# Optimization experiments

Measured on AMD Instinct MI355X. Metric: run time of the kernel, lower is better.

## Reference

```python
import jax, jax.numpy as jnp
import numpy as np


def setup_inputs() -> dict:
    key = jax.random.key(0)
    ks = jax.random.split(key, 7)
    B, N, Fin, Fout = 32, 1024, 64, 64
    s = 1.0 / np.sqrt(Fin)
    return {
        "X": jax.random.normal(ks[0], (B, N, Fin), dtype=jnp.float32),
        "A": jax.random.normal(ks[1], (B, N, N), dtype=jnp.float32),  # unused in forward, kept for signature fidelity
        "W": jax.random.uniform(ks[2], (Fin, Fout), jnp.float32, -s, s),
        "att_W": jax.random.uniform(ks[3], (Fin, Fout), jnp.float32, -s, s),
        "a": jax.random.uniform(ks[4], (Fout, Fout), jnp.float32, -s, s),
        "bias_W": jax.random.uniform(ks[5], (Fout,), jnp.float32, -s, s),
        "self_W": jax.random.uniform(ks[6], (Fin, Fout), jnp.float32, -s, s),
    }


def reference(X, A, W, att_W, a, bias_W, self_W):
    # att_X = X @ att_W : [B, N, Fout]
    att_X = jnp.einsum('bnf,fg->bng', X, att_W)
    # torch einsum 'ij,ajk->ajk' sums `a` over i => per-feature scale a.sum(0)
    scale = jnp.sum(a, axis=0)  # [Fout]
    # Z[b,i,k] = sum_j att_X[b,i,j] * scale[j] * att_X[b,k,j]  -> [B, N, N]
    Z = jnp.einsum('big,bkg->bik', att_X * scale, att_X)
    n = Z.shape[1]
    Z = Z * (1.0 - jnp.eye(n, dtype=Z.dtype))  # zero diagonal per batch
    att = jax.nn.leaky_relu(Z, negative_slope=0.01)
    # H = att @ (X W) + bias_W + X self_W
    XW = jnp.einsum('bnf,fg->bng', X, W)
    H = jnp.einsum('bnm,bmg->bng', att, XW) + bias_W
    H = H + jnp.einsum('bnf,fg->bng', X, self_W)
    return H
```

## Files before the change

### kernel.cpp

```cpp
#include <hip/hip_runtime.h>

#define DEV __device__ __forceinline__
typedef short s16x8 __attribute__((ext_vector_type(8)));
typedef float f32x16 __attribute__((ext_vector_type(16)));
typedef unsigned short u16;

#define WAIT_VMCNT(N) asm volatile("s_waitcnt vmcnt(" #N ")" ::: "memory")
#define CFENCE asm volatile("" ::: "memory")

DEV unsigned cvt_pk_bf16(float lo, float hi) {
  unsigned r;
  asm volatile("v_cvt_pk_bf16_f32 %0, %1, %2" : "=v"(r) : "v"(lo), "v"(hi));
  return r;
}
DEV u16 f2bf(float f) {
  unsigned u = __builtin_bit_cast(unsigned, f);
  unsigned r = u + 0x7fffu + ((u >> 16) & 1u);
  return (u16)(r >> 16);
}
DEV float bf2f(u16 u) { return __builtin_bit_cast(float, (unsigned)u << 16); }
DEV f32x16 zero16() {
  f32x16 v;
  #pragma unroll
  for (int i = 0; i < 16; ++i) v[i] = 0.f;
  return v;
}

DEV void gld16(const u16* g, u16* l) {
  __builtin_amdgcn_global_load_lds(
      (const __attribute__((address_space(1))) void*)g,
      (__attribute__((address_space(3))) void*)l, 16, 0, 0);
}

DEV void stage_tile64(const u16* __restrict__ gbase, size_t stride, u16* lbuf, int t) {
  #pragma unroll
  for (int p = 0; p < 2; ++p) {
    int c = p * 256 + t;
    int row = c >> 3, s = c & 7;
    int gck = s ^ (row & 7);
    const u16* src = gbase + (size_t)row * stride + gck * 8;
    u16* dst = lbuf + (size_t)(p * 256 + (t & 192)) * 8;
    gld16(src, dst);
  }
}

DEV s16x8 frag(const u16* buf, int row, int chunk) {
  return *(const s16x8*)(buf + row * 64 + ((chunk ^ (row & 7)) << 3));
}

DEV int kswz(int row, int d) {
  return row * 64 + ((((d >> 3) ^ (row & 7)) << 3) | (d & 7));
}

DEV void stage_wt(const float* __restrict__ src, u16* dst, int t) {
  #pragma unroll
  for (int r = 0; r < 4; ++r) {
    int e = (r * 256 + t) * 4;
    int f = e >> 6, g0 = e & 63;
    float4 v = *(const float4*)(src + f * 64 + g0);
    float vv[4] = {v.x, v.y, v.z, v.w};
    #pragma unroll
    for (int j = 0; j < 4; ++j) {
      int g = g0 + j;
      dst[g * 64 + ((((f >> 3) ^ (g & 7)) << 3) | (f & 7))] = f2bf(vv[j]);
    }
  }
}

__global__ __launch_bounds__(256) void prep_kernel(
    const float* __restrict__ X, const float* __restrict__ W,
    const float* __restrict__ attW, const float* __restrict__ Aa,
    const float* __restrict__ biasW, const float* __restrict__ selfW,
    u16* __restrict__ Kbf, u16* __restrict__ Vt, u16* __restrict__ Bb,
    float* __restrict__ scal_ws) {
  __shared__ __align__(16) u16 Xl[64 * 64];
  __shared__ __align__(16) u16 Wt[3][64 * 64];
  __shared__ __align__(16) u16 Bl[64 * 64];
  __shared__ __align__(16) u16 Vl[64 * 72];
  __shared__ float sc4[4][64];

  const int t = threadIdx.x;
  const int r0 = blockIdx.x * 64;
  const int b = r0 >> 10;
  const int n0 = r0 & 1023;

  if (blockIdx.x == 0) {
    int qt = t >> 6, d = t & 63;
    float s = 0.f;
    #pragma unroll
    for (int i = 0; i < 16; ++i) s += Aa[(qt * 16 + i) * 64 + d];
    sc4[qt][d] = s;
  }

  #pragma unroll
  for (int p = 0; p < 2; ++p) {
    int c = p * 256 + t;
    int row = c >> 3, ck = c & 7;
    const float4* src = (const float4*)(X + (size_t)(r0 + row) * 64 + ck * 8);
    float4 a0 = src[0], a1 = src[1];
    unsigned* dst = (unsigned*)&Xl[row * 64 + ((ck ^ (row & 7)) << 3)];
    dst[0] = cvt_pk_bf16(a0.x, a0.y);
    dst[1] = cvt_pk_bf16(a0.z, a0.w);
    dst[2] = cvt_pk_bf16(a1.x, a1.y);
    dst[3] = cvt_pk_bf16(a1.z, a1.w);
  }
  stage_wt(attW, &Wt[0][0], t);
  stage_wt(W, &Wt[1][0], t);
  stage_wt(selfW, &Wt[2][0], t);
  __syncthreads();

  const int lane = t & 63, w = t >> 6, h = lane >> 5, ln = lane & 31;
  const int rg = (w >> 1) * 32;
  const int cf = w & 1;
  const int d = cf * 32 + ln;

  s16x8 xa[4];
  #pragma unroll
  for (int ks = 0; ks < 4; ++ks) xa[ks] = frag(Xl, rg + ln, ks * 2 + h);

  f32x16 aA = zero16(), aW = zero16(), aS = zero16();
  #pragma unroll
  for (int ks = 0; ks < 4; ++ks) {
    s16x8 bA = frag(&Wt[0][0], d, ks * 2 + h);
    s16x8 bW = frag(&Wt[1][0], d, ks * 2 + h);
    s16x8 bS = frag(&Wt[2][0], d, ks * 2 + h);
    aA = __builtin_amdgcn_mfma_f32_32x32x16_bf16(xa[ks], bA, aA, 0, 0, 0);
    aW = __builtin_amdgcn_mfma_f32_32x32x16_bf16(xa[ks], bW, aW, 0, 0, 0);
    aS = __builtin_amdgcn_mfma_f32_32x32x16_bf16(xa[ks], bS, aS, 0, 0, 0);
  }
  __syncthreads();

  const float bi = biasW[d];
  #pragma unroll
  for (int reg = 0; reg < 16; ++reg) {
    int rl = (reg & 3) + 8 * (reg >> 2) + 4 * h;
    int row = rg + rl;
    Xl[kswz(row, d)] = f2bf(aA[reg]);
    Bl[kswz(row, d)] = f2bf(aS[reg] + bi);
  }
  #pragma unroll
  for (int pg = 0; pg < 4; ++pg) {
    int n = rg + pg * 8 + 4 * h;
    *(unsigned*)&Vl[d * 72 + n] = cvt_pk_bf16(aW[pg * 4 + 0], aW[pg * 4 + 1]);
    *(unsigned*)&Vl[d * 72 + n + 2] = cvt_pk_bf16(aW[pg * 4 + 2], aW[pg * 4 + 3]);
  }
  __syncthreads();

  #pragma unroll
  for (int p = 0; p < 2; ++p) {
    int c = p * 256 + t;
    int row = c >> 3, ck = c & 7;
    size_t go = (size_t)(r0 + row) * 64 + ck * 8;
    *(s16x8*)&Kbf[go] = *(const s16x8*)&Xl[row * 64 + ((ck ^ (row & 7)) << 3)];
    *(s16x8*)&Bb[go] = *(const s16x8*)&Bl[row * 64 + ((ck ^ (row & 7)) << 3)];
  }
  #pragma unroll
  for (int p = 0; p < 2; ++p) {
    int c = p * 256 + t;
    int dd = c >> 3, ck = c & 7;
    *(s16x8*)&Vt[(size_t)(b * 64 + dd) * 1024 + n0 + ck * 8] =
        *(const s16x8*)&Vl[dd * 72 + ck * 8];
  }
  if (blockIdx.x == 0 && t < 64)
    scal_ws[t] = sc4[0][t] + sc4[1][t] + sc4[2][t] + sc4[3][t];
}

#define PROC(SV, DG, PWV)                                                      \
  do {                                                                         \
    float p_[16];                                                              \
    _Pragma("unroll") for (int r_ = 0; r_ < 16; ++r_) {                        \
      float v_ = (SV)[r_];                                                     \
      p_[r_] = fmaxf(v_, 0.f) + 0.01f * fminf(v_, 0.f);                        \
    }                                                                          \
    if (DG) {                                                                  \
      _Pragma("unroll") for (int r_ = 0; r_ < 16; ++r_) {                      \
        int rl_ = (r_ & 3) + 8 * (r_ >> 2) + 4 * h;                            \
        p_[r_] = (rl_ == ln) ? 0.f : p_[r_];                                   \
      }                                                                        \
    }                                                                          \
    unsigned pk_[8];                                                           \
    _Pragma("unroll") for (int i_ = 0; i_ < 8; ++i_)                           \
        pk_[i_] = cvt_pk_bf16(p_[2 * i_], p_[2 * i_ + 1]);                     \
    auto a0_ = __builtin_amdgcn_permlane32_swap(pk_[0], pk_[2], false, false); \
    auto a1_ = __builtin_amdgcn_permlane32_swap(pk_[1], pk_[3], false, false); \
    auto a2_ = __builtin_amdgcn_permlane32_swap(pk_[4], pk_[6], false, false); \
    auto a3_ = __builtin_amdgcn_permlane32_swap(pk_[5], pk_[7], false, false); \
    PWV[0][0] = a0_[0]; PWV[0][1] = a1_[0]; PWV[0][2] = a0_[1];                \
    PWV[0][3] = a1_[1]; PWV[1][0] = a2_[0]; PWV[1][1] = a3_[0];                \
    PWV[1][2] = a2_[1]; PWV[1][3] = a3_[1];                                    \
  } while (0)

__global__ __launch_bounds__(256) void attn_kernel(
    const u16* __restrict__ Kbf, const u16* __restrict__ Vt,
    const u16* __restrict__ Bb, const float* __restrict__ scal_ws,
    float* __restrict__ Hout) {
  __shared__ __align__(16) u16 KV[4][2][64 * 64];
  __shared__ float sc[64];
  float* Ol0 = (float*)&KV[0][0][0];
  float* Ol1 = (float*)&KV[1][0][0];

  const int t = threadIdx.x;
  const int b = blockIdx.x;
  const int q0 = blockIdx.y * 64;
  const int lane = t & 63, w = t >> 6, h = lane >> 5, ln = lane & 31;
  const int qh = w & 1, kvh = w >> 1;
  const int qg = q0 + qh * 32 + ln;

  const u16* Kg = Kbf + (size_t)b * 65536;
  const u16* Vg = Vt + (size_t)b * 65536;

  s16x8 qraw[4];
  #pragma unroll
  for (int ks = 0; ks < 4; ++ks)
    qraw[ks] = *(const s16x8*)(Kg + (size_t)qg * 64 + ks * 16 + h * 8);
  float scv = 0.f;
  if (t < 64) scv = scal_ws[t];

  stage_tile64(Kg, 64, &KV[0][0][0], t);
  stage_tile64(Vg, 1024, &KV[0][1][0], t);
  stage_tile64(Kg + (size_t)64 * 64, 64, &KV[1][0][0], t);
  stage_tile64(Vg + 64, 1024, &KV[1][1][0], t);

  if (t < 64) sc[t] = scv;
  asm volatile("s_waitcnt lgkmcnt(0)" ::: "memory");
  __builtin_amdgcn_s_barrier();
  CFENCE;

  s16x8 qf[4];
  #pragma unroll
  for (int ks = 0; ks < 4; ++ks) {
    float4 s0 = *(const float4*)&sc[ks * 16 + h * 8];
    float4 s1 = *(const float4*)&sc[ks * 16 + h * 8 + 4];
    union { unsigned u[4]; s16x8 v; } qq;
    qq.u[0] = cvt_pk_bf16(bf2f((u16)qraw[ks][0]) * s0.x, bf2f((u16)qraw[ks][1]) * s0.y);
    qq.u[1] = cvt_pk_bf16(bf2f((u16)qraw[ks][2]) * s0.z, bf2f((u16)qraw[ks][3]) * s0.w);
    qq.u[2] = cvt_pk_bf16(bf2f((u16)qraw[ks][4]) * s1.x, bf2f((u16)qraw[ks][5]) * s1.y);
    qq.u[3] = cvt_pk_bf16(bf2f((u16)qraw[ks][6]) * s1.z, bf2f((u16)qraw[ks][7]) * s1.w);
    qf[ks] = qq.v;
  }

  f32x16 o0 = zero16(), o1 = zero16();

  #pragma unroll 1
  for (int tix = 0; tix < 16; ++tix) {
    const int kv0 = tix * 64;
    if (tix < 14) {
      const int ns = (tix + 2) & 3;
      stage_tile64(Kg + (size_t)(kv0 + 128) * 64, 64, &KV[ns][0][0], t);
      stage_tile64(Vg + (kv0 + 128), 1024, &KV[ns][1][0], t);
      WAIT_VMCNT(8);
    } else if (tix == 14) {
      WAIT_VMCNT(4);
    } else {
      WAIT_VMCNT(0);
    }
    __builtin_amdgcn_s_barrier();
    CFENCE;
    const u16* Kl = &KV[tix & 3][0][0];
    const u16* Vl = &KV[tix & 3][1][0];

    f32x16 s = zero16();
    __builtin_amdgcn_s_setprio(1);
    #pragma unroll
    for (int ks = 0; ks < 4; ++ks)
      s = __builtin_amdgcn_mfma_f32_32x32x16_bf16(frag(Kl, kvh * 32 + ln, ks * 2 + h), qf[ks], s, 0, 0, 0);
    __builtin_amdgcn_s_setprio(0);

    const bool dg = (kv0 + kvh * 32) == (q0 + qh * 32);
    unsigned pw[2][4];
    PROC(s, dg, pw);

    __builtin_amdgcn_s_setprio(1);
    #pragma unroll
    for (int kk = 0; kk < 2; ++kk) {
      union { unsigned u[4]; s16x8 v; } pb;
      pb.u[0] = pw[kk][0]; pb.u[1] = pw[kk][1];
      pb.u[2] = pw[kk][2]; pb.u[3] = pw[kk][3];
      int ch = kvh * 4 + kk * 2 + h;
      o0 = __builtin_amdgcn_mfma_f32_32x32x16_bf16(frag(Vl, ln, ch), pb.v, o0, 0, 0, 0);
      o1 = __builtin_amdgcn_mfma_f32_32x32x16_bf16(frag(Vl, 32 + ln, ch), pb.v, o1, 0, 0, 0);
    }
    __builtin_amdgcn_s_setprio(0);
  }

  float* Od = kvh ? Ol1 : Ol0;
  const int q = qh * 32 + ln;
  #pragma unroll
  for (int reg = 0; reg < 16; ++reg) {
    int rl = (reg & 3) + 8 * (reg >> 2) + 4 * h;
    int d0 = rl, d1 = 32 + rl;
    Od[q * 64 + ((((d0 >> 2) ^ (q & 15)) << 2) | (d0 & 3))] = o0[reg];
    Od[q * 64 + ((((d1 >> 2) ^ (q & 15)) << 2) | (d1 & 3))] = o1[reg];
  }
  __syncthreads();
  #pragma unroll
  for (int i = 0; i < 4; ++i) {
    int fi = i * 256 + t;
    int qq = fi >> 4, g = fi & 15;
    int off = qq * 64 + ((g ^ (qq & 15)) << 2);
    float4 v0 = *(const float4*)&Ol0[off];
    float4 v1 = *(const float4*)&Ol1[off];
    size_t go = ((size_t)b * 1024 + q0 + qq) * 64 + g * 4;
    const short4 bv = *(const short4*)(Bb + go);
    float4 v;
    v.x = v0.x + v1.x + bf2f((u16)bv.x);
    v.y = v0.y + v1.y + bf2f((u16)bv.y);
    v.z = v0.z + v1.z + bf2f((u16)bv.z);
    v.w = v0.w + v1.w + bf2f((u16)bv.w);
    *(float4*)(Hout + go) = v;
  }
}

extern "C" void kernel_launch(void* const* d_in, const int* in_sizes, int n_in,
                              void* d_out, int out_size, void* d_ws, size_t ws_size,
                              hipStream_t stream) {
  const float* X = (const float*)d_in[0];
  const float* W = (const float*)d_in[2];
  const float* attW = (const float*)d_in[3];
  const float* a = (const float*)d_in[4];
  const float* biasW = (const float*)d_in[5];
  const float* selfW = (const float*)d_in[6];
  float* H = (float*)d_out;

  u16* Kbf = (u16*)d_ws;
  u16* Vt = Kbf + (size_t)32 * 1024 * 64;
  u16* Bb = Vt + (size_t)32 * 1024 * 64;
  float* scal = (float*)(Bb + (size_t)32 * 1024 * 64);

  prep_kernel<<<512, 256, 0, stream>>>(X, W, attW, a, biasW, selfW, Kbf, Vt, Bb, scal);
  attn_kernel<<<dim3(32, 16), 256, 0, stream>>>(Kbf, Vt, Bb, scal, H);
}
```

Measured before the change: 35.63 us.

## Precompute weights and scaled Q in prep kernels, use 3-stage KV ring

```diff
diff --git a/kernel.cpp b/kernel.cpp
--- a/kernel.cpp
+++ b/kernel.cpp
@@ -52,45 +52,69 @@
   return row * 64 + ((((d >> 3) ^ (row & 7)) << 3) | (d & 7));
 }
 
-DEV void stage_wt(const float* __restrict__ src, u16* dst, int t) {
-  #pragma unroll
-  for (int r = 0; r < 4; ++r) {
-    int e = (r * 256 + t) * 4;
-    int f = e >> 6, g0 = e & 63;
-    float4 v = *(const float4*)(src + f * 64 + g0);
-    float vv[4] = {v.x, v.y, v.z, v.w};
-    #pragma unroll
-    for (int j = 0; j < 4; ++j) {
-      int g = g0 + j;
-      dst[g * 64 + ((((f >> 3) ^ (g & 7)) << 3) | (f & 7))] = f2bf(vv[j]);
-    }
-  }
-}
-
-__global__ __launch_bounds__(256) void prep_kernel(
-    const float* __restrict__ X, const float* __restrict__ W,
-    const float* __restrict__ attW, const float* __restrict__ Aa,
-    const float* __restrict__ biasW, const float* __restrict__ selfW,
-    u16* __restrict__ Kbf, u16* __restrict__ Vt, u16* __restrict__ Bb,
-    float* __restrict__ scal_ws) {
-  __shared__ __align__(16) u16 Xl[64 * 64];
-  __shared__ __align__(16) u16 Wt[3][64 * 64];
-  __shared__ __align__(16) u16 Bl[64 * 64];
-  __shared__ __align__(16) u16 Vl[64 * 72];
+__global__ __launch_bounds__(256) void wprep_kernel(
+    const float* __restrict__ attW, const float* __restrict__ W,
+    const float* __restrict__ selfW, const float* __restrict__ Aa,
+    u16* __restrict__ Wsw, float* __restrict__ scal_ws) {
+  __shared__ __align__(16) u16 T[64 * 72];
   __shared__ float sc4[4][64];
-
-  const int t = threadIdx.x;
-  const int r0 = blockIdx.x * 64;
-  const int b = r0 >> 10;
-  const int n0 = r0 & 1023;
-
-  if (blockIdx.x == 0) {
+  const int t = threadIdx.x, bi = blockIdx.x;
+
+  if (bi == 0) {
     int qt = t >> 6, d = t & 63;
     float s = 0.f;
     #pragma unroll
     for (int i = 0; i < 16; ++i) s += Aa[(qt * 16 + i) * 64 + d];
     sc4[qt][d] = s;
   }
+
+  const float* src = (bi == 0) ? attW : (bi == 1) ? W : selfW;
+  #pragma unroll
+  for (int p = 0; p < 4; ++p) {
+    int c = p * 256 + t;
+    int f = c >> 4, g0 = (c & 15) * 4;
+    float4 v = *(const float4*)(src + f * 64 + g0);
+    T[(g0 + 0) * 72 + f] = f2bf(v.x);
+    T[(g0 + 1) * 72 + f] = f2bf(v.y);
+    T[(g0 + 2) * 72 + f] = f2bf(v.z);
+    T[(g0 + 3) * 72 + f] = f2bf(v.w);
+  }
+  __syncthreads();
+  #pragma unroll
+  for (int p = 0; p < 2; ++p) {
+    int c = p * 256 + t;
+    int g = c >> 3, f0 = (c & 7) * 8;
+    *(s16x8*)&Wsw[bi * 4096 + g * 64 + f0] = *(const s16x8*)&T[g * 72 + f0];
+  }
+  if (bi == 0 && t < 64)
+    scal_ws[t] = sc4[0][t] + sc4[1][t] + sc4[2][t] + sc4[3][t];
+}
+
+__global__ __launch_bounds__(256) void prep_kernel(
+    const float* __restrict__ X, const u16* __restrict__ Wsw,
+    const float* __restrict__ scal_ws, const float* __restrict__ biasW,
+    u16* __restrict__ Kbf, u16* __restrict__ Qbf, u16* __restrict__ Vt,
+    u16* __restrict__ Bb) {
+  __shared__ __align__(16) u16 Xl[64 * 64];
+  __shared__ __align__(16) u16 WtL[3][64 * 64];
+  __shared__ __align__(16) u16 Ql[64 * 64];
+  __shared__ __align__(16) u16 Bl[64 * 64];
+  __shared__ __align__(16) u16 Vl[64 * 72];
+
+  const int t = threadIdx.x;
+  const int r0 = blockIdx.x * 64;
+  const int b = r0 >> 10;
+  const int n0 = r0 & 1023;
+  const int lane = t & 63, w = t >> 6, h = lane >> 5, ln = lane & 31;
+  const int rg = (w >> 1) * 32;
+  const int cf = w & 1;
+  const int d = cf * 32 + ln;
+
+  #pragma unroll
+  for (int i = 0; i < 3; ++i) stage_tile64(Wsw + i * 4096, 64, &WtL[i][0], t);
+
+  const float sc_d = scal_ws[d];
+  const float bi = biasW[d];
 
   #pragma unroll
   for (int p = 0; p < 2; ++p) {
@@ -104,15 +128,7 @@
     dst[2] = cvt_pk_bf16(a1.x, a1.y);
     dst[3] = cvt_pk_bf16(a1.z, a1.w);
   }
-  stage_wt(attW, &Wt[0][0], t);
-  stage_wt(W, &Wt[1][0], t);
-  stage_wt(selfW, &Wt[2][0], t);
-  __syncthreads();
-
-  const int lane = t & 63, w = t >> 6, h = lane >> 5, ln = lane & 31;
-  const int rg = (w >> 1) * 32;
-  const int cf = w & 1;
-  const int d = cf * 32 + ln;
+  __syncthreads();
 
   s16x8 xa[4];
   #pragma unroll
@@ -121,21 +137,21 @@
   f32x16 aA = zero16(), aW = zero16(), aS = zero16();
   #pragma unroll
   for (int ks = 0; ks < 4; ++ks) {
-    s16x8 bA = frag(&Wt[0][0], d, ks * 2 + h);
-    s16x8 bW = frag(&Wt[1][0], d, ks * 2 + h);
-    s16x8 bS = frag(&Wt[2][0], d, ks * 2 + h);
+    s16x8 bA = frag(&WtL[0][0], d, ks * 2 + h);
+    s16x8 bW = frag(&WtL[1][0], d, ks * 2 + h);
+    s16x8 bS = frag(&WtL[2][0], d, ks * 2 + h);
     aA = __builtin_amdgcn_mfma_f32_32x32x16_bf16(xa[ks], bA, aA, 0, 0, 0);
     aW = __builtin_amdgcn_mfma_f32_32x32x16_bf16(xa[ks], bW, aW, 0, 0, 0);
     aS = __builtin_amdgcn_mfma_f32_32x32x16_bf16(xa[ks], bS, aS, 0, 0, 0);
   }
   __syncthreads();
 
-  const float bi = biasW[d];
   #pragma unroll
   for (int reg = 0; reg < 16; ++reg) {
     int rl = (reg & 3) + 8 * (reg >> 2) + 4 * h;
     int row = rg + rl;
     Xl[kswz(row, d)] = f2bf(aA[reg]);
+    Ql[kswz(row, d)] = f2bf(aA[reg] * sc_d);
     Bl[kswz(row, d)] = f2bf(aS[reg] + bi);
   }
   #pragma unroll
@@ -151,8 +167,10 @@
     int c = p * 256 + t;
     int row = c >> 3, ck = c & 7;
     size_t go = (size_t)(r0 + row) * 64 + ck * 8;
-    *(s16x8*)&Kbf[go] = *(const s16x8*)&Xl[row * 64 + ((ck ^ (row & 7)) << 3)];
-    *(s16x8*)&Bb[go] = *(const s16x8*)&Bl[row * 64 + ((ck ^ (row & 7)) << 3)];
+    int lo = row * 64 + ((ck ^ (row & 7)) << 3);
+    *(s16x8*)&Kbf[go] = *(const s16x8*)&Xl[lo];
+    *(s16x8*)&Qbf[go] = *(const s16x8*)&Ql[lo];
+    *(s16x8*)&Bb[go] = *(const s16x8*)&Bl[lo];
   }
   #pragma unroll
   for (int p = 0; p < 2; ++p) {
@@ -161,8 +179,6 @@
     *(s16x8*)&Vt[(size_t)(b * 64 + dd) * 1024 + n0 + ck * 8] =
         *(const s16x8*)&Vl[dd * 72 + ck * 8];
   }
-  if (blockIdx.x == 0 && t < 64)
-    scal_ws[t] = sc4[0][t] + sc4[1][t] + sc4[2][t] + sc4[3][t];
 }
 
 #define PROC(SV, DG, PWV)                                                      \
@@ -191,11 +207,10 @@
   } while (0)
 
 __global__ __launch_bounds__(256) void attn_kernel(
-    const u16* __restrict__ Kbf, const u16* __restrict__ Vt,
-    const u16* __restrict__ Bb, const float* __restrict__ scal_ws,
+    const u16* __restrict__ Qbf, const u16* __restrict__ Kbf,
+    const u16* __restrict__ Vt, const u16* __restrict__ Bb,
     float* __restrict__ Hout) {
-  __shared__ __align__(16) u16 KV[4][2][64 * 64];
-  __shared__ float sc[64];
+  __shared__ __align__(16) u16 KV[3][2][64 * 64];
   float* Ol0 = (float*)&KV[0][0][0];
   float* Ol1 = (float*)&KV[1][0][0];
 
@@ -206,58 +221,39 @@
   const int qh = w & 1, kvh = w >> 1;
   const int qg = q0 + qh * 32 + ln;
 
+  const u16* Qg = Qbf + (size_t)b * 65536;
   const u16* Kg = Kbf + (size_t)b * 65536;
   const u16* Vg = Vt + (size_t)b * 65536;
 
-  s16x8 qraw[4];
+  s16x8 qf[4];
   #pragma unroll
   for (int ks = 0; ks < 4; ++ks)
-    qraw[ks] = *(const s16x8*)(Kg + (size_t)qg * 64 + ks * 16 + h * 8);
-  float scv = 0.f;
-  if (t < 64) scv = scal_ws[t];
+    qf[ks] = *(const s16x8*)(Qg + (size_t)qg * 64 + ks * 16 + h * 8);
 
   stage_tile64(Kg, 64, &KV[0][0][0], t);
   stage_tile64(Vg, 1024, &KV[0][1][0], t);
   stage_tile64(Kg + (size_t)64 * 64, 64, &KV[1][0][0], t);
   stage_tile64(Vg + 64, 1024, &KV[1][1][0], t);
 
-  if (t < 64) sc[t] = scv;
-  asm volatile("s_waitcnt lgkmcnt(0)" ::: "memory");
-  __builtin_amdgcn_s_barrier();
-  CFENCE;
-
-  s16x8 qf[4];
-  #pragma unroll
-  for (int ks = 0; ks < 4; ++ks) {
-    float4 s0 = *(const float4*)&sc[ks * 16 + h * 8];
-    float4 s1 = *(const float4*)&sc[ks * 16 + h * 8 + 4];
-    union { unsigned u[4]; s16x8 v; } qq;
-    qq.u[0] = cvt_pk_bf16(bf2f((u16)qraw[ks][0]) * s0.x, bf2f((u16)qraw[ks][1]) * s0.y);
-    qq.u[1] = cvt_pk_bf16(bf2f((u16)qraw[ks][2]) * s0.z, bf2f((u16)qraw[ks][3]) * s0.w);
-    qq.u[2] = cvt_pk_bf16(bf2f((u16)qraw[ks][4]) * s1.x, bf2f((u16)qraw[ks][5]) * s1.y);
-    qq.u[3] = cvt_pk_bf16(bf2f((u16)qraw[ks][6]) * s1.z, bf2f((u16)qraw[ks][7]) * s1.w);
-    qf[ks] = qq.v;
-  }
-
   f32x16 o0 = zero16(), o1 = zero16();
 
   #pragma unroll 1
   for (int tix = 0; tix < 16; ++tix) {
     const int kv0 = tix * 64;
-    if (tix < 14) {
-      const int ns = (tix + 2) & 3;
-      stage_tile64(Kg + (size_t)(kv0 + 128) * 64, 64, &KV[ns][0][0], t);
-      stage_tile64(Vg + (kv0 + 128), 1024, &KV[ns][1][0], t);
-      WAIT_VMCNT(8);
-    } else if (tix == 14) {
+    if (tix < 15) {
       WAIT_VMCNT(4);
     } else {
       WAIT_VMCNT(0);
     }
     __builtin_amdgcn_s_barrier();
     CFENCE;
-    const u16* Kl = &KV[tix & 3][0][0];
-    const u16* Vl = &KV[tix & 3][1][0];
+    if (tix < 14) {
+      const int ns = (tix + 2) % 3;
+      stage_tile64(Kg + (size_t)(kv0 + 128) * 64, 64, &KV[ns][0][0], t);
+      stage_tile64(Vg + (kv0 + 128), 1024, &KV[ns][1][0], t);
+    }
+    const u16* Kl = &KV[tix % 3][0][0];
+    const u16* Vl = &KV[tix % 3][1][0];
 
     f32x16 s = zero16();
     __builtin_amdgcn_s_setprio(1);
@@ -282,6 +278,8 @@
     }
     __builtin_amdgcn_s_setprio(0);
   }
+
+  __syncthreads();
 
   float* Od = kvh ? Ol1 : Ol0;
   const int q = qh * 32 + ln;
@@ -323,10 +321,13 @@
   float* H = (float*)d_out;
 
   u16* Kbf = (u16*)d_ws;
-  u16* Vt = Kbf + (size_t)32 * 1024 * 64;
+  u16* Qbf = Kbf + (size_t)32 * 1024 * 64;
+  u16* Vt = Qbf + (size_t)32 * 1024 * 64;
   u16* Bb = Vt + (size_t)32 * 1024 * 64;
-  float* scal = (float*)(Bb + (size_t)32 * 1024 * 64);
-
-  prep_kernel<<<512, 256, 0, stream>>>(X, W, attW, a, biasW, selfW, Kbf, Vt, Bb, scal);
-  attn_kernel<<<dim3(32, 16), 256, 0, stream>>>(Kbf, Vt, Bb, scal, H);
-}
+  u16* Wsw = Bb + (size_t)32 * 1024 * 64;
+  float* scal = (float*)(Wsw + 3 * 4096);
+
+  wprep_kernel<<<3, 256, 0, stream>>>(attW, W, selfW, a, Wsw, scal);
+  prep_kernel<<<512, 256, 0, stream>>>(X, Wsw, scal, biasW, Kbf, Qbf, Vt, Bb);
+  attn_kernel<<<dim3(32, 16), 256, 0, stream>>>(Qbf, Kbf, Vt, Bb, H);
+}
```

Result: slower. 37.72 us (+5.9%).

## Give each attention wave its own 32 queries over full KV tiles, 128 queries per block

Applied to the files above, without the earlier changes.

```diff
diff --git a/kernel.cpp b/kernel.cpp
--- a/kernel.cpp
+++ b/kernel.cpp
@@ -80,16 +80,21 @@
   __shared__ float sc4[4][64];
 
   const int t = threadIdx.x;
-  const int r0 = blockIdx.x * 64;
-  const int b = r0 >> 10;
-  const int n0 = r0 & 1023;
-
-  if (blockIdx.x == 0) {
-    int qt = t >> 6, d = t & 63;
+  const int b = blockIdx.x;
+  const int n0 = blockIdx.y * 64;
+  const int r0 = b * 1024 + n0;
+  const bool sblk = (blockIdx.x == 0 && blockIdx.y == 0);
+  const int lane = t & 63, w = t >> 6, h = lane >> 5, ln = lane & 31;
+  const int rg = (w >> 1) * 32;
+  const int cf = w & 1;
+  const int d = cf * 32 + ln;
+
+  if (sblk) {
+    int qt = t >> 6, dd = t & 63;
     float s = 0.f;
     #pragma unroll
-    for (int i = 0; i < 16; ++i) s += Aa[(qt * 16 + i) * 64 + d];
-    sc4[qt][d] = s;
+    for (int i = 0; i < 16; ++i) s += Aa[(qt * 16 + i) * 64 + dd];
+    sc4[qt][dd] = s;
   }
 
   #pragma unroll
@@ -109,11 +114,6 @@
   stage_wt(selfW, &Wt[2][0], t);
   __syncthreads();
 
-  const int lane = t & 63, w = t >> 6, h = lane >> 5, ln = lane & 31;
-  const int rg = (w >> 1) * 32;
-  const int cf = w & 1;
-  const int d = cf * 32 + ln;
-
   s16x8 xa[4];
   #pragma unroll
   for (int ks = 0; ks < 4; ++ks) xa[ks] = frag(Xl, rg + ln, ks * 2 + h);
@@ -151,8 +151,9 @@
     int c = p * 256 + t;
     int row = c >> 3, ck = c & 7;
     size_t go = (size_t)(r0 + row) * 64 + ck * 8;
-    *(s16x8*)&Kbf[go] = *(const s16x8*)&Xl[row * 64 + ((ck ^ (row & 7)) << 3)];
-    *(s16x8*)&Bb[go] = *(const s16x8*)&Bl[row * 64 + ((ck ^ (row & 7)) << 3)];
+    int lo = row * 64 + ((ck ^ (row & 7)) << 3);
+    *(s16x8*)&Kbf[go] = *(const s16x8*)&Xl[lo];
+    *(s16x8*)&Bb[go] = *(const s16x8*)&Bl[lo];
   }
   #pragma unroll
   for (int p = 0; p < 2; ++p) {
@@ -161,7 +162,7 @@
     *(s16x8*)&Vt[(size_t)(b * 64 + dd) * 1024 + n0 + ck * 8] =
         *(const s16x8*)&Vl[dd * 72 + ck * 8];
   }
-  if (blockIdx.x == 0 && t < 64)
+  if (sblk && t < 64)
     scal_ws[t] = sc4[0][t] + sc4[1][t] + sc4[2][t] + sc4[3][t];
 }
 
@@ -194,48 +195,33 @@
     const u16* __restrict__ Kbf, const u16* __restrict__ Vt,
     const u16* __restrict__ Bb, const float* __restrict__ scal_ws,
     float* __restrict__ Hout) {
-  __shared__ __align__(16) u16 KV[4][2][64 * 64];
-  __shared__ float sc[64];
-  float* Ol0 = (float*)&KV[0][0][0];
-  float* Ol1 = (float*)&KV[1][0][0];
+  __shared__ __align__(16) u16 ring[3][2][4096];
 
   const int t = threadIdx.x;
   const int b = blockIdx.x;
-  const int q0 = blockIdx.y * 64;
+  const int q0 = blockIdx.y * 128;
   const int lane = t & 63, w = t >> 6, h = lane >> 5, ln = lane & 31;
-  const int qh = w & 1, kvh = w >> 1;
-  const int qg = q0 + qh * 32 + ln;
+  const int qb = q0 + w * 32;
 
   const u16* Kg = Kbf + (size_t)b * 65536;
   const u16* Vg = Vt + (size_t)b * 65536;
 
-  s16x8 qraw[4];
-  #pragma unroll
-  for (int ks = 0; ks < 4; ++ks)
-    qraw[ks] = *(const s16x8*)(Kg + (size_t)qg * 64 + ks * 16 + h * 8);
-  float scv = 0.f;
-  if (t < 64) scv = scal_ws[t];
-
-  stage_tile64(Kg, 64, &KV[0][0][0], t);
-  stage_tile64(Vg, 1024, &KV[0][1][0], t);
-  stage_tile64(Kg + (size_t)64 * 64, 64, &KV[1][0][0], t);
-  stage_tile64(Vg + 64, 1024, &KV[1][1][0], t);
-
-  if (t < 64) sc[t] = scv;
-  asm volatile("s_waitcnt lgkmcnt(0)" ::: "memory");
-  __builtin_amdgcn_s_barrier();
-  CFENCE;
+  stage_tile64(Kg, 64, &ring[0][0][0], t);
+  stage_tile64(Vg, 1024, &ring[0][1][0], t);
+  stage_tile64(Kg + (size_t)64 * 64, 64, &ring[1][0][0], t);
+  stage_tile64(Vg + 64, 1024, &ring[1][1][0], t);
 
   s16x8 qf[4];
   #pragma unroll
   for (int ks = 0; ks < 4; ++ks) {
-    float4 s0 = *(const float4*)&sc[ks * 16 + h * 8];
-    float4 s1 = *(const float4*)&sc[ks * 16 + h * 8 + 4];
+    s16x8 raw = *(const s16x8*)(Kg + (size_t)(qb + ln) * 64 + ks * 16 + h * 8);
+    float4 sA = *(const float4*)(scal_ws + ks * 16 + h * 8);
+    float4 sB = *(const float4*)(scal_ws + ks * 16 + h * 8 + 4);
     union { unsigned u[4]; s16x8 v; } qq;
-    qq.u[0] = cvt_pk_bf16(bf2f((u16)qraw[ks][0]) * s0.x, bf2f((u16)qraw[ks][1]) * s0.y);
-    qq.u[1] = cvt_pk_bf16(bf2f((u16)qraw[ks][2]) * s0.z, bf2f((u16)qraw[ks][3]) * s0.w);
-    qq.u[2] = cvt_pk_bf16(bf2f((u16)qraw[ks][4]) * s1.x, bf2f((u16)qraw[ks][5]) * s1.y);
-    qq.u[3] = cvt_pk_bf16(bf2f((u16)qraw[ks][6]) * s1.z, bf2f((u16)qraw[ks][7]) * s1.w);
+    qq.u[0] = cvt_pk_bf16(bf2f((u16)raw[0]) * sA.x, bf2f((u16)raw[1]) * sA.y);
+    qq.u[1] = cvt_pk_bf16(bf2f((u16)raw[2]) * sA.z, bf2f((u16)raw[3]) * sA.w);
+    qq.u[2] = cvt_pk_bf16(bf2f((u16)raw[4]) * sB.x, bf2f((u16)raw[5]) * sB.y);
+    qq.u[3] = cvt_pk_bf16(bf2f((u16)raw[6]) * sB.z, bf2f((u16)raw[7]) * sB.w);
     qf[ks] = qq.v;
   }
 
@@ -244,69 +230,72 @@
   #pragma unroll 1
   for (int tix = 0; tix < 16; ++tix) {
     const int kv0 = tix * 64;
-    if (tix < 14) {
-      const int ns = (tix + 2) & 3;
-      stage_tile64(Kg + (size_t)(kv0 + 128) * 64, 64, &KV[ns][0][0], t);
-      stage_tile64(Vg + (kv0 + 128), 1024, &KV[ns][1][0], t);
-      WAIT_VMCNT(8);
-    } else if (tix == 14) {
+    if (tix < 15) {
       WAIT_VMCNT(4);
     } else {
       WAIT_VMCNT(0);
     }
     __builtin_amdgcn_s_barrier();
     CFENCE;
-    const u16* Kl = &KV[tix & 3][0][0];
-    const u16* Vl = &KV[tix & 3][1][0];
-
-    f32x16 s = zero16();
+    if (tix < 14) {
+      const int ns = (tix + 2) % 3;
+      stage_tile64(Kg + (size_t)(kv0 + 128) * 64, 64, &ring[ns][0][0], t);
+      stage_tile64(Vg + (kv0 + 128), 1024, &ring[ns][1][0], t);
+    }
+    const u16* Kl = &ring[tix % 3][0][0];
+    const u16* Vl = &ring[tix % 3][1][0];
+
+    f32x16 s0 = zero16(), s1 = zero16();
     __builtin_amdgcn_s_setprio(1);
     #pragma unroll
-    for (int ks = 0; ks < 4; ++ks)
-      s = __builtin_amdgcn_mfma_f32_32x32x16_bf16(frag(Kl, kvh * 32 + ln, ks * 2 + h), qf[ks], s, 0, 0, 0);
+    for (int ks = 0; ks < 4; ++ks) {
+      s0 = __builtin_amdgcn_mfma_f32_32x32x16_bf16(frag(Kl, ln, ks * 2 + h), qf[ks], s0, 0, 0, 0);
+      s1 = __builtin_amdgcn_mfma_f32_32x32x16_bf16(frag(Kl, 32 + ln, ks * 2 + h), qf[ks], s1, 0, 0, 0);
+    }
     __builtin_amdgcn_s_setprio(0);
 
-    const bool dg = (kv0 + kvh * 32) == (q0 + qh * 32);
-    unsigned pw[2][4];
-    PROC(s, dg, pw);
+    const bool dg0 = (kv0 == qb);
+    const bool dg1 = (kv0 + 32 == qb);
+    unsigned pw0[2][4], pw1[2][4];
+    PROC(s0, dg0, pw0);
+    PROC(s1, dg1, pw1);
 
     __builtin_amdgcn_s_setprio(1);
     #pragma unroll
-    for (int kk = 0; kk < 2; ++kk) {
+    for (int c = 0; c < 4; ++c) {
       union { unsigned u[4]; s16x8 v; } pb;
-      pb.u[0] = pw[kk][0]; pb.u[1] = pw[kk][1];
-      pb.u[2] = pw[kk][2]; pb.u[3] = pw[kk][3];
-      int ch = kvh * 4 + kk * 2 + h;
-      o0 = __builtin_amdgcn_mfma_f32_32x32x16_bf16(frag(Vl, ln, ch), pb.v, o0, 0, 0, 0);
-      o1 = __builtin_amdgcn_mfma_f32_32x32x16_bf16(frag(Vl, 32 + ln, ch), pb.v, o1, 0, 0, 0);
+      pb.u[0] = (c < 2 ? pw0 : pw1)[c & 1][0];
+      pb.u[1] = (c < 2 ? pw0 : pw1)[c & 1][1];
+      pb.u[2] = (c < 2 ? pw0 : pw1)[c & 1][2];
+      pb.u[3] = (c < 2 ? pw0 : pw1)[c & 1][3];
+      o0 = __builtin_amdgcn_mfma_f32_32x32x16_bf16(frag(Vl, ln, c * 2 + h), pb.v, o0, 0, 0, 0);
+      o1 = __builtin_amdgcn_mfma_f32_32x32x16_bf16(frag(Vl, 32 + ln, c * 2 + h), pb.v, o1, 0, 0, 0);
     }
     __builtin_amdgcn_s_setprio(0);
   }
 
-  float* Od = kvh ? Ol1 : Ol0;
-  const int q = qh * 32 + ln;
+  __syncthreads();
+
+  float* Ow = (float*)&ring[0][0][0] + (size_t)w * 2048;
   #pragma unroll
   for (int reg = 0; reg < 16; ++reg) {
     int rl = (reg & 3) + 8 * (reg >> 2) + 4 * h;
     int d0 = rl, d1 = 32 + rl;
-    Od[q * 64 + ((((d0 >> 2) ^ (q & 15)) << 2) | (d0 & 3))] = o0[reg];
-    Od[q * 64 + ((((d1 >> 2) ^ (q & 15)) << 2) | (d1 & 3))] = o1[reg];
-  }
-  __syncthreads();
-  #pragma unroll
-  for (int i = 0; i < 4; ++i) {
-    int fi = i * 256 + t;
-    int qq = fi >> 4, g = fi & 15;
-    int off = qq * 64 + ((g ^ (qq & 15)) << 2);
-    float4 v0 = *(const float4*)&Ol0[off];
-    float4 v1 = *(const float4*)&Ol1[off];
-    size_t go = ((size_t)b * 1024 + q0 + qq) * 64 + g * 4;
+    Ow[ln * 64 + ((((d0 >> 2) ^ (ln & 15)) << 2) | (d0 & 3))] = o0[reg];
+    Ow[ln * 64 + ((((d1 >> 2) ^ (ln & 15)) << 2) | (d1 & 3))] = o1[reg];
+  }
+  #pragma unroll
+  for (int p = 0; p < 8; ++p) {
+    int row = p * 4 + (lane >> 4);
+    int g = lane & 15;
+    int off = row * 64 + ((g ^ (row & 15)) << 2);
+    float4 v = *(const float4*)&Ow[off];
+    size_t go = ((size_t)b * 1024 + qb + row) * 64 + g * 4;
     const short4 bv = *(const short4*)(Bb + go);
-    float4 v;
-    v.x = v0.x + v1.x + bf2f((u16)bv.x);
-    v.y = v0.y + v1.y + bf2f((u16)bv.y);
-    v.z = v0.z + v1.z + bf2f((u16)bv.z);
-    v.w = v0.w + v1.w + bf2f((u16)bv.w);
+    v.x += bf2f((u16)bv.x);
+    v.y += bf2f((u16)bv.y);
+    v.z += bf2f((u16)bv.z);
+    v.w += bf2f((u16)bv.w);
     *(float4*)(Hout + go) = v;
   }
 }
@@ -327,6 +316,7 @@
   u16* Bb = Vt + (size_t)32 * 1024 * 64;
   float* scal = (float*)(Bb + (size_t)32 * 1024 * 64);
 
-  prep_kernel<<<512, 256, 0, stream>>>(X, W, attW, a, biasW, selfW, Kbf, Vt, Bb, scal);
-  attn_kernel<<<dim3(32, 16), 256, 0, stream>>>(Kbf, Vt, Bb, scal, H);
-}
+  prep_kernel<<<dim3(32, 16), 256, 0, stream>>>(X, W, attW, a, biasW, selfW,
+                                                Kbf, Vt, Bb, scal);
+  attn_kernel<<<dim3(32, 8), 256, 0, stream>>>(Kbf, Vt, Bb, scal, H);
+}
```

Measured after the change: 34.39 us. 3.5% less time.

## Fuse prep and attention kernels with a global atomic grid barrier

Applied to the files above, without the earlier changes.

```diff
diff --git a/kernel.cpp b/kernel.cpp
--- a/kernel.cpp
+++ b/kernel.cpp
@@ -52,117 +52,18 @@
   return row * 64 + ((((d >> 3) ^ (row & 7)) << 3) | (d & 7));
 }
 
-DEV void stage_wt(const float* __restrict__ src, u16* dst, int t) {
-  #pragma unroll
-  for (int r = 0; r < 4; ++r) {
-    int e = (r * 256 + t) * 4;
-    int f = e >> 6, g0 = e & 63;
-    float4 v = *(const float4*)(src + f * 64 + g0);
-    float vv[4] = {v.x, v.y, v.z, v.w};
-    #pragma unroll
-    for (int j = 0; j < 4; ++j) {
-      int g = g0 + j;
-      dst[g * 64 + ((((f >> 3) ^ (g & 7)) << 3) | (f & 7))] = f2bf(vv[j]);
-    }
-  }
-}
-
-__global__ __launch_bounds__(256) void prep_kernel(
-    const float* __restrict__ X, const float* __restrict__ W,
-    const float* __restrict__ attW, const float* __restrict__ Aa,
-    const float* __restrict__ biasW, const float* __restrict__ selfW,
-    u16* __restrict__ Kbf, u16* __restrict__ Vt, u16* __restrict__ Bb,
-    float* __restrict__ scal_ws) {
-  __shared__ __align__(16) u16 Xl[64 * 64];
-  __shared__ __align__(16) u16 Wt[3][64 * 64];
-  __shared__ __align__(16) u16 Bl[64 * 64];
-  __shared__ __align__(16) u16 Vl[64 * 72];
-  __shared__ float sc4[4][64];
-
-  const int t = threadIdx.x;
-  const int r0 = blockIdx.x * 64;
-  const int b = r0 >> 10;
-  const int n0 = r0 & 1023;
-
-  if (blockIdx.x == 0) {
-    int qt = t >> 6, d = t & 63;
-    float s = 0.f;
-    #pragma unroll
-    for (int i = 0; i < 16; ++i) s += Aa[(qt * 16 + i) * 64 + d];
-    sc4[qt][d] = s;
-  }
-
+DEV void stage_wt2(const float* __restrict__ src, u16* dst, int t) {
+  const int g = t & 63, kk = t >> 6;
   #pragma unroll
   for (int p = 0; p < 2; ++p) {
-    int c = p * 256 + t;
-    int row = c >> 3, ck = c & 7;
-    const float4* src = (const float4*)(X + (size_t)(r0 + row) * 64 + ck * 8);
-    float4 a0 = src[0], a1 = src[1];
-    unsigned* dst = (unsigned*)&Xl[row * 64 + ((ck ^ (row & 7)) << 3)];
-    dst[0] = cvt_pk_bf16(a0.x, a0.y);
-    dst[1] = cvt_pk_bf16(a0.z, a0.w);
-    dst[2] = cvt_pk_bf16(a1.x, a1.y);
-    dst[3] = cvt_pk_bf16(a1.z, a1.w);
-  }
-  stage_wt(attW, &Wt[0][0], t);
-  stage_wt(W, &Wt[1][0], t);
-  stage_wt(selfW, &Wt[2][0], t);
-  __syncthreads();
-
-  const int lane = t & 63, w = t >> 6, h = lane >> 5, ln = lane & 31;
-  const int rg = (w >> 1) * 32;
-  const int cf = w & 1;
-  const int d = cf * 32 + ln;
-
-  s16x8 xa[4];
-  #pragma unroll
-  for (int ks = 0; ks < 4; ++ks) xa[ks] = frag(Xl, rg + ln, ks * 2 + h);
-
-  f32x16 aA = zero16(), aW = zero16(), aS = zero16();
-  #pragma unroll
-  for (int ks = 0; ks < 4; ++ks) {
-    s16x8 bA = frag(&Wt[0][0], d, ks * 2 + h);
-    s16x8 bW = frag(&Wt[1][0], d, ks * 2 + h);
-    s16x8 bS = frag(&Wt[2][0], d, ks * 2 + h);
-    aA = __builtin_amdgcn_mfma_f32_32x32x16_bf16(xa[ks], bA, aA, 0, 0, 0);
-    aW = __builtin_amdgcn_mfma_f32_32x32x16_bf16(xa[ks], bW, aW, 0, 0, 0);
-    aS = __builtin_amdgcn_mfma_f32_32x32x16_bf16(xa[ks], bS, aS, 0, 0, 0);
-  }
-  __syncthreads();
-
-  const float bi = biasW[d];
-  #pragma unroll
-  for (int reg = 0; reg < 16; ++reg) {
-    int rl = (reg & 3) + 8 * (reg >> 2) + 4 * h;
-    int row = rg + rl;
-    Xl[kswz(row, d)] = f2bf(aA[reg]);
-    Bl[kswz(row, d)] = f2bf(aS[reg] + bi);
-  }
-  #pragma unroll
-  for (int pg = 0; pg < 4; ++pg) {
-    int n = rg + pg * 8 + 4 * h;
-    *(unsigned*)&Vl[d * 72 + n] = cvt_pk_bf16(aW[pg * 4 + 0], aW[pg * 4 + 1]);
-    *(unsigned*)&Vl[d * 72 + n + 2] = cvt_pk_bf16(aW[pg * 4 + 2], aW[pg * 4 + 3]);
-  }
-  __syncthreads();
-
-  #pragma unroll
-  for (int p = 0; p < 2; ++p) {
-    int c = p * 256 + t;
-    int row = c >> 3, ck = c & 7;
-    size_t go = (size_t)(r0 + row) * 64 + ck * 8;
-    *(s16x8*)&Kbf[go] = *(const s16x8*)&Xl[row * 64 + ((ck ^ (row & 7)) << 3)];
-    *(s16x8*)&Bb[go] = *(const s16x8*)&Bl[row * 64 + ((ck ^ (row & 7)) << 3)];
-  }
-  #pragma unroll
-  for (int p = 0; p < 2; ++p) {
-    int c = p * 256 + t;
-    int dd = c >> 3, ck = c & 7;
-    *(s16x8*)&Vt[(size_t)(b * 64 + dd) * 1024 + n0 + ck * 8] =
-        *(const s16x8*)&Vl[dd * 72 + ck * 8];
-  }
-  if (blockIdx.x == 0 && t < 64)
-    scal_ws[t] = sc4[0][t] + sc4[1][t] + sc4[2][t] + sc4[3][t];
+    const int k8 = kk + p * 4;
+    union { unsigned u[4]; s16x8 v; } pk;
+    #pragma unroll
+    for (int j = 0; j < 4; ++j)
+      pk.u[j] = cvt_pk_bf16(src[(k8 * 8 + 2 * j) * 64 + g],
+                            src[(k8 * 8 + 2 * j + 1) * 64 + g]);
+    *(s16x8*)&dst[g * 64 + ((k8 ^ (g & 7)) << 3)] = pk.v;
+  }
 }
 
 #define PROC(SV, DG, PWV)                                                      \
@@ -190,124 +91,228 @@
     PWV[1][2] = a2_[1]; PWV[1][3] = a3_[1];                                    \
   } while (0)
 
-__global__ __launch_bounds__(256) void attn_kernel(
-    const u16* __restrict__ Kbf, const u16* __restrict__ Vt,
-    const u16* __restrict__ Bb, const float* __restrict__ scal_ws,
+__global__ __launch_bounds__(256) void fused_kernel(
+    const float* __restrict__ X, const float* __restrict__ W,
+    const float* __restrict__ attW, const float* __restrict__ Aa,
+    const float* __restrict__ biasW, const float* __restrict__ selfW,
+    u16* __restrict__ Kbf, u16* __restrict__ Vt, u16* __restrict__ Bb,
+    float* __restrict__ scal_ws, unsigned* __restrict__ cnt,
     float* __restrict__ Hout) {
-  __shared__ __align__(16) u16 KV[4][2][64 * 64];
-  __shared__ float sc[64];
-  float* Ol0 = (float*)&KV[0][0][0];
-  float* Ol1 = (float*)&KV[1][0][0];
+  __shared__ __align__(16) u16 smem[25088];
+  __shared__ float sc4[4][64];
 
   const int t = threadIdx.x;
-  const int b = blockIdx.x;
-  const int q0 = blockIdx.y * 64;
+  const int id = blockIdx.x;
+  const int b = id & 31;
+  const int nt = id >> 5;
+  const int n0 = nt * 64;
+  const int r0 = b * 1024 + n0;
   const int lane = t & 63, w = t >> 6, h = lane >> 5, ln = lane & 31;
-  const int qh = w & 1, kvh = w >> 1;
-  const int qg = q0 + qh * 32 + ln;
-
-  const u16* Kg = Kbf + (size_t)b * 65536;
-  const u16* Vg = Vt + (size_t)b * 65536;
-
-  s16x8 qraw[4];
-  #pragma unroll
-  for (int ks = 0; ks < 4; ++ks)
-    qraw[ks] = *(const s16x8*)(Kg + (size_t)qg * 64 + ks * 16 + h * 8);
-  float scv = 0.f;
-  if (t < 64) scv = scal_ws[t];
-
-  stage_tile64(Kg, 64, &KV[0][0][0], t);
-  stage_tile64(Vg, 1024, &KV[0][1][0], t);
-  stage_tile64(Kg + (size_t)64 * 64, 64, &KV[1][0][0], t);
-  stage_tile64(Vg + 64, 1024, &KV[1][1][0], t);
-
-  if (t < 64) sc[t] = scv;
-  asm volatile("s_waitcnt lgkmcnt(0)" ::: "memory");
-  __builtin_amdgcn_s_barrier();
-  CFENCE;
-
-  s16x8 qf[4];
-  #pragma unroll
-  for (int ks = 0; ks < 4; ++ks) {
-    float4 s0 = *(const float4*)&sc[ks * 16 + h * 8];
-    float4 s1 = *(const float4*)&sc[ks * 16 + h * 8 + 4];
-    union { unsigned u[4]; s16x8 v; } qq;
-    qq.u[0] = cvt_pk_bf16(bf2f((u16)qraw[ks][0]) * s0.x, bf2f((u16)qraw[ks][1]) * s0.y);
-    qq.u[1] = cvt_pk_bf16(bf2f((u16)qraw[ks][2]) * s0.z, bf2f((u16)qraw[ks][3]) * s0.w);
-    qq.u[2] = cvt_pk_bf16(bf2f((u16)qraw[ks][4]) * s1.x, bf2f((u16)qraw[ks][5]) * s1.y);
-    qq.u[3] = cvt_pk_bf16(bf2f((u16)qraw[ks][6]) * s1.z, bf2f((u16)qraw[ks][7]) * s1.w);
-    qf[ks] = qq.v;
-  }
-
-  f32x16 o0 = zero16(), o1 = zero16();
-
-  #pragma unroll 1
-  for (int tix = 0; tix < 16; ++tix) {
-    const int kv0 = tix * 64;
-    if (tix < 14) {
-      const int ns = (tix + 2) & 3;
-      stage_tile64(Kg + (size_t)(kv0 + 128) * 64, 64, &KV[ns][0][0], t);
-      stage_tile64(Vg + (kv0 + 128), 1024, &KV[ns][1][0], t);
-      WAIT_VMCNT(8);
-    } else if (tix == 14) {
-      WAIT_VMCNT(4);
-    } else {
-      WAIT_VMCNT(0);
-    }
-    __builtin_amdgcn_s_barrier();
-    CFENCE;
-    const u16* Kl = &KV[tix & 3][0][0];
-    const u16* Vl = &KV[tix & 3][1][0];
-
-    f32x16 s = zero16();
-    __builtin_amdgcn_s_setprio(1);
+
+  {
+    u16* Xl = smem;
+    u16* Wt0 = smem + 4096;
+    u16* Wt1 = smem + 8192;
+    u16* Wt2 = smem + 12288;
+    u16* Bl = smem + 16384;
+    u16* Vl = smem + 20480;
+
+    if (id == 0) {
+      int qt = t >> 6, dd = t & 63;
+      float s = 0.f;
+      #pragma unroll
+      for (int i = 0; i < 16; ++i) s += Aa[(qt * 16 + i) * 64 + dd];
+      sc4[qt][dd] = s;
+    }
+
+    #pragma unroll
+    for (int p = 0; p < 2; ++p) {
+      int c = p * 256 + t;
+      int row = c >> 3, ck = c & 7;
+      const float4* src = (const float4*)(X + (size_t)(r0 + row) * 64 + ck * 8);
+      float4 a0 = src[0], a1 = src[1];
+      unsigned* dst = (unsigned*)&Xl[row * 64 + ((ck ^ (row & 7)) << 3)];
+      dst[0] = cvt_pk_bf16(a0.x, a0.y);
+      dst[1] = cvt_pk_bf16(a0.z, a0.w);
+      dst[2] = cvt_pk_bf16(a1.x, a1.y);
+      dst[3] = cvt_pk_bf16(a1.z, a1.w);
+    }
+    stage_wt2(attW, Wt0, t);
+    stage_wt2(W, Wt1, t);
+    stage_wt2(selfW, Wt2, t);
+    __syncthreads();
+
+    const int rg = (w >> 1) * 32;
+    const int cf = w & 1;
+    const int d = cf * 32 + ln;
+
+    s16x8 xa[4];
+    #pragma unroll
+    for (int ks = 0; ks < 4; ++ks) xa[ks] = frag(Xl, rg + ln, ks * 2 + h);
+
+    f32x16 aA = zero16(), aW = zero16(), aS = zero16();
+    #pragma unroll
+    for (int ks = 0; ks < 4; ++ks) {
+      s16x8 bA = frag(Wt0, d, ks * 2 + h);
+      s16x8 bW = frag(Wt1, d, ks * 2 + h);
+      s16x8 bS = frag(Wt2, d, ks * 2 + h);
+      aA = __builtin_amdgcn_mfma_f32_32x32x16_bf16(xa[ks], bA, aA, 0, 0, 0);
+      aW = __builtin_amdgcn_mfma_f32_32x32x16_bf16(xa[ks], bW, aW, 0, 0, 0);
+      aS = __builtin_amdgcn_mfma_f32_32x32x16_bf16(xa[ks], bS, aS, 0, 0, 0);
+    }
+    __syncthreads();
+
+    const float bi = biasW[d];
+    #pragma unroll
+    for (int reg = 0; reg < 16; ++reg) {
+      int rl = (reg & 3) + 8 * (reg >> 2) + 4 * h;
+      int row = rg + rl;
+      Xl[kswz(row, d)] = f2bf(aA[reg]);
+      Bl[kswz(row, d)] = f2bf(aS[reg] + bi);
+    }
+    #pragma unroll
+    for (int pg = 0; pg < 4; ++pg) {
+      int n = rg + pg * 8 + 4 * h;
+      *(unsigned*)&Vl[d * 72 + n] = cvt_pk_bf16(aW[pg * 4 + 0], aW[pg * 4 + 1]);
+      *(unsigned*)&Vl[d * 72 + n + 2] = cvt_pk_bf16(aW[pg * 4 + 2], aW[pg * 4 + 3]);
+    }
+    __syncthreads();
+
+    #pragma unroll
+    for (int p = 0; p < 2; ++p) {
+      int c = p * 256 + t;
+      int row = c >> 3, ck = c & 7;
+      size_t go = (size_t)(r0 + row) * 64 + ck * 8;
+      int lo = row * 64 + ((ck ^ (row & 7)) << 3);
+      *(s16x8*)&Kbf[go] = *(const s16x8*)&Xl[lo];
+      *(s16x8*)&Bb[go] = *(const s16x8*)&Bl[lo];
+    }
+    #pragma unroll
+    for (int p = 0; p < 2; ++p) {
+      int c = p * 256 + t;
+      int dd = c >> 3, ck = c & 7;
+      *(s16x8*)&Vt[(size_t)(b * 64 + dd) * 1024 + n0 + ck * 8] =
+          *(const s16x8*)&Vl[dd * 72 + ck * 8];
+    }
+    if (id == 0 && t < 64)
+      scal_ws[t] = sc4[0][t] + sc4[1][t] + sc4[2][t] + sc4[3][t];
+  }
+
+  __syncthreads();
+  if (t == 0) {
+    __threadfence();
+    __hip_atomic_fetch_add(cnt, 1u, __ATOMIC_ACQ_REL, __HIP_MEMORY_SCOPE_AGENT);
+    while (__hip_atomic_load(cnt, __ATOMIC_ACQUIRE, __HIP_MEMORY_SCOPE_AGENT) < 512u)
+      __builtin_amdgcn_s_sleep(8);
+  }
+  __syncthreads();
+  __threadfence();
+
+  {
+    const int q0 = n0;
+    const int qh = w & 1, kvh = w >> 1;
+    const u16* Kg = Kbf + (size_t)b * 65536;
+    const u16* Vg = Vt + (size_t)b * 65536;
+
+    const int qrow = q0 + qh * 32 + ln;
+    s16x8 raw[4];
     #pragma unroll
     for (int ks = 0; ks < 4; ++ks)
-      s = __builtin_amdgcn_mfma_f32_32x32x16_bf16(frag(Kl, kvh * 32 + ln, ks * 2 + h), qf[ks], s, 0, 0, 0);
-    __builtin_amdgcn_s_setprio(0);
-
-    const bool dg = (kv0 + kvh * 32) == (q0 + qh * 32);
-    unsigned pw[2][4];
-    PROC(s, dg, pw);
-
-    __builtin_amdgcn_s_setprio(1);
-    #pragma unroll
-    for (int kk = 0; kk < 2; ++kk) {
-      union { unsigned u[4]; s16x8 v; } pb;
-      pb.u[0] = pw[kk][0]; pb.u[1] = pw[kk][1];
-      pb.u[2] = pw[kk][2]; pb.u[3] = pw[kk][3];
-      int ch = kvh * 4 + kk * 2 + h;
-      o0 = __builtin_amdgcn_mfma_f32_32x32x16_bf16(frag(Vl, ln, ch), pb.v, o0, 0, 0, 0);
-      o1 = __builtin_amdgcn_mfma_f32_32x32x16_bf16(frag(Vl, 32 + ln, ch), pb.v, o1, 0, 0, 0);
-    }
-    __builtin_amdgcn_s_setprio(0);
-  }
-
-  float* Od = kvh ? Ol1 : Ol0;
-  const int q = qh * 32 + ln;
-  #pragma unroll
-  for (int reg = 0; reg < 16; ++reg) {
-    int rl = (reg & 3) + 8 * (reg >> 2) + 4 * h;
-    int d0 = rl, d1 = 32 + rl;
-    Od[q * 64 + ((((d0 >> 2) ^ (q & 15)) << 2) | (d0 & 3))] = o0[reg];
-    Od[q * 64 + ((((d1 >> 2) ^ (q & 15)) << 2) | (d1 & 3))] = o1[reg];
-  }
-  __syncthreads();
-  #pragma unroll
-  for (int i = 0; i < 4; ++i) {
-    int fi = i * 256 + t;
-    int qq = fi >> 4, g = fi & 15;
-    int off = qq * 64 + ((g ^ (qq & 15)) << 2);
-    float4 v0 = *(const float4*)&Ol0[off];
-    float4 v1 = *(const float4*)&Ol1[off];
-    size_t go = ((size_t)b * 1024 + q0 + qq) * 64 + g * 4;
-    const short4 bv = *(const short4*)(Bb + go);
-    float4 v;
-    v.x = v0.x + v1.x + bf2f((u16)bv.x);
-    v.y = v0.y + v1.y + bf2f((u16)bv.y);
-    v.z = v0.z + v1.z + bf2f((u16)bv.z);
-    v.w = v0.w + v1.w + bf2f((u16)bv.w);
-    *(float4*)(Hout + go) = v;
+      raw[ks] = *(const s16x8*)(Kg + (size_t)qrow * 64 + ks * 16 + h * 8);
+
+    stage_tile64(Kg, 64, smem, t);
+    stage_tile64(Vg, 1024, smem + 4096, t);
+    stage_tile64(Kg + (size_t)64 * 64, 64, smem + 8192, t);
+    stage_tile64(Vg + 64, 1024, smem + 12288, t);
+
+    s16x8 qf[4];
+    #pragma unroll
+    for (int ks = 0; ks < 4; ++ks) {
+      float4 sA = *(const float4*)(scal_ws + ks * 16 + h * 8);
+      float4 sB = *(const float4*)(scal_ws + ks * 16 + h * 8 + 4);
+      union { unsigned u[4]; s16x8 v; } qq;
+      qq.u[0] = cvt_pk_bf16(bf2f((u16)raw[ks][0]) * sA.x, bf2f((u16)raw[ks][1]) * sA.y);
+      qq.u[1] = cvt_pk_bf16(bf2f((u16)raw[ks][2]) * sA.z, bf2f((u16)raw[ks][3]) * sA.w);
+      qq.u[2] = cvt_pk_bf16(bf2f((u16)raw[ks][4]) * sB.x, bf2f((u16)raw[ks][5]) * sB.y);
+      qq.u[3] = cvt_pk_bf16(bf2f((u16)raw[ks][6]) * sB.z, bf2f((u16)raw[ks][7]) * sB.w);
+      qf[ks] = qq.v;
+    }
+
+    f32x16 o0 = zero16(), o1 = zero16();
+
+    #pragma unroll 1
+    for (int tix = 0; tix < 16; ++tix) {
+      const int kv0 = tix * 64;
+      if (tix < 15) {
+        WAIT_VMCNT(4);
+      } else {
+        WAIT_VMCNT(0);
+      }
+      __builtin_amdgcn_s_barrier();
+      CFENCE;
+      if (tix < 14) {
+        const int ns = (tix + 2) % 3;
+        stage_tile64(Kg + (size_t)(kv0 + 128) * 64, 64, smem + ns * 8192, t);
+        stage_tile64(Vg + (kv0 + 128), 1024, smem + ns * 8192 + 4096, t);
+      }
+      const u16* Kl = smem + (tix % 3) * 8192;
+      const u16* Vl = Kl + 4096;
+
+      f32x16 s = zero16();
+      __builtin_amdgcn_s_setprio(1);
+      #pragma unroll
+      for (int ks = 0; ks < 4; ++ks)
+        s = __builtin_amdgcn_mfma_f32_32x32x16_bf16(
+            frag(Kl, kvh * 32 + ln, ks * 2 + h), qf[ks], s, 0, 0, 0);
+      __builtin_amdgcn_s_setprio(0);
+
+      const bool dg = (kv0 + kvh * 32) == (q0 + qh * 32);
+      unsigned pw[2][4];
+      PROC(s, dg, pw);
+
+      __builtin_amdgcn_s_setprio(1);
+      #pragma unroll
+      for (int kk = 0; kk < 2; ++kk) {
+        union { unsigned u[4]; s16x8 v; } pb;
+        pb.u[0] = pw[kk][0]; pb.u[1] = pw[kk][1];
+        pb.u[2] = pw[kk][2]; pb.u[3] = pw[kk][3];
+        int ch = kvh * 4 + kk * 2 + h;
+        o0 = __builtin_amdgcn_mfma_f32_32x32x16_bf16(frag(Vl, ln, ch), pb.v, o0, 0, 0, 0);
+        o1 = __builtin_amdgcn_mfma_f32_32x32x16_bf16(frag(Vl, 32 + ln, ch), pb.v, o1, 0, 0, 0);
+      }
+      __builtin_amdgcn_s_setprio(0);
+    }
+
+    __syncthreads();
+
+    float* Ol0 = (float*)smem;
+    float* Ol1 = (float*)(smem + 8192);
+    float* Od = kvh ? Ol1 : Ol0;
+    const int q = qh * 32 + ln;
+    #pragma unroll
+    for (int reg = 0; reg < 16; ++reg) {
+      int rl = (reg & 3) + 8 * (reg >> 2) + 4 * h;
+      int d0 = rl, d1 = 32 + rl;
+      Od[q * 64 + ((((d0 >> 2) ^ (q & 15)) << 2) | (d0 & 3))] = o0[reg];
+      Od[q * 64 + ((((d1 >> 2) ^ (q & 15)) << 2) | (d1 & 3))] = o1[reg];
+    }
+    __syncthreads();
+    #pragma unroll
+    for (int i = 0; i < 4; ++i) {
+      int fi = i * 256 + t;
+      int qq = fi >> 4, g = fi & 15;
+      int off = qq * 64 + ((g ^ (qq & 15)) << 2);
+      float4 v0 = *(const float4*)&Ol0[off];
+      float4 v1 = *(const float4*)&Ol1[off];
+      size_t go = ((size_t)b * 1024 + q0 + qq) * 64 + g * 4;
+      const short4 bv = *(const short4*)(Bb + go);
+      float4 v;
+      v.x = v0.x + v1.x + bf2f((u16)bv.x);
+      v.y = v0.y + v1.y + bf2f((u16)bv.y);
+      v.z = v0.z + v1.z + bf2f((u16)bv.z);
+      v.w = v0.w + v1.w + bf2f((u16)bv.w);
+      *(float4*)(Hout + go) = v;
+    }
   }
 }
 
@@ -326,7 +331,9 @@
   u16* Vt = Kbf + (size_t)32 * 1024 * 64;
   u16* Bb = Vt + (size_t)32 * 1024 * 64;
   float* scal = (float*)(Bb + (size_t)32 * 1024 * 64);
-
-  prep_kernel<<<512, 256, 0, stream>>>(X, W, attW, a, biasW, selfW, Kbf, Vt, Bb, scal);
-  attn_kernel<<<dim3(32, 16), 256, 0, stream>>>(Kbf, Vt, Bb, scal, H);
-}
+  unsigned* cnt = (unsigned*)(scal + 64);
+
+  hipMemsetAsync(cnt, 0, 4, stream);
+  fused_kernel<<<512, 256, 0, stream>>>(X, W, attW, a, biasW, selfW,
+                                        Kbf, Vt, Bb, scal, cnt, H);
+}
```

Result: slower. 116.2 us (+226.1%).
